# Kernel optimization log

Hardware: AMD Instinct MI355X
Metric: run time of the kernel (lower is better)

Reference implementation:

```python
import math
import jax, jax.numpy as jnp
import numpy as np


def setup_inputs() -> dict:
    key = jax.random.key(0)
    ks = jax.random.split(key, 8)
    N, Lv, M, Lt = 4096, 16, 4096, 77
    Din, D, R = 512, 768, 4  # fc in-dim, model dim, bottleneck ratio
    Dh = D // R
    s = lambda k, shape, fan_in: jax.random.normal(k, shape, jnp.float32) * (1.0 / math.sqrt(fan_in))
    return {
        "vision_prompt": jax.random.normal(ks[0], (N, Lv, D), jnp.float32),
        "text_prompt": jax.random.normal(ks[1], (M, Lt, Din), jnp.float32),
        "fc_w": s(ks[2], (D, Din), Din),        # torch Linear layout [out, in]
        "fc_b": jnp.zeros((D,), jnp.float32),
        "ln_g": jnp.ones((D,), jnp.float32),
        "ln_b": jnp.zeros((D,), jnp.float32),
        "mlp_w1": s(ks[3], (Dh, D), D),
        "mlp_b1": jnp.zeros((Dh,), jnp.float32),
        "mlp_w2": s(ks[4], (D, Dh), Dh),
        "mlp_b2": jnp.zeros((D,), jnp.float32),
    }


def _layernorm(x, g, b, eps=1e-5):
    mu = jnp.mean(x, axis=-1, keepdims=True)
    var = jnp.var(x, axis=-1, keepdims=True)
    return (x - mu) * jax.lax.rsqrt(var + eps) * g + b


def reference(vision_prompt, text_prompt, fc_w, fc_b, ln_g, ln_b,
              mlp_w1, mlp_b1, mlp_w2, mlp_b2):
    N, Lv, D = vision_prompt.shape
    mean_v = jnp.mean(vision_prompt, axis=1)                    # [N, D]
    mean_t = jnp.mean(text_prompt, axis=1)                      # [M, Din]
    t = mean_t @ fc_w.T + fc_b                                  # [M, D]
    scores = jnp.einsum('nc,mc->nm', mean_v, t) / math.sqrt(D)  # [N, M]
    aff = jax.nn.softmax(scores, axis=-1)
    agg = jnp.einsum('nm,mc->nc', aff, t)                       # [N, D]
    h = _layernorm(agg, ln_g, ln_b)
    h = jax.nn.relu(h @ mlp_w1.T + mlp_b1)
    h = h @ mlp_w2.T + mlp_b2                                   # [N, D]
    return jnp.broadcast_to(h[:, None, :], (N, Lv, D))
```

## Files before the change

### kernel.cpp

```cpp
#include <hip/hip_runtime.h>
#include <math.h>

typedef unsigned short u16;
typedef __attribute__((ext_vector_type(4))) float f32x4;
typedef __attribute__((ext_vector_type(8))) short bf16x8;

#define GLOBAL_AS __attribute__((address_space(1)))
#define LDS_AS __attribute__((address_space(3)))

__device__ __forceinline__ u16 f2bf(float f) {
  unsigned u = __builtin_bit_cast(unsigned, f);
  unsigned lsb = (u >> 16) & 1u;
  u += 0x7fffu + lsb;
  return (u16)(u >> 16);
}

__device__ __forceinline__ float bf2f(u16 b) {
  return __builtin_bit_cast(float, ((unsigned)b) << 16);
}

__device__ __forceinline__ void gload16(const void* g, void* l) {
  __builtin_amdgcn_global_load_lds((const GLOBAL_AS void*)g, (LDS_AS void*)l, 16, 0, 0);
}

__global__ __launch_bounds__(256) void prologue_kernel(
    const float* __restrict__ vision, const float* __restrict__ text,
    const float* __restrict__ fc_w, const float* __restrict__ w1,
    const float* __restrict__ w2, const float* __restrict__ b1,
    u16* __restrict__ mean_v, u16* __restrict__ mean_t,
    u16* __restrict__ fcw_bf, u16* __restrict__ w1p, u16* __restrict__ w2p,
    float* __restrict__ b1p)
{
  const int n_mv = 4096 * 192;
  const int n_mt = 4096 * 128;
  const int n_fcw = 768 * 512;
  const int n_w1 = 256 * 768;
  const int n_w2 = 768 * 256;
  int id = blockIdx.x * 256 + threadIdx.x;

  if (id < n_mv) {
    int n = id / 192, c = id % 192;
    const f32x4* x = (const f32x4*)vision + (size_t)n * 16 * 192 + c;
    f32x4 s = {0.f, 0.f, 0.f, 0.f};
#pragma unroll
    for (int l = 0; l < 16; ++l) s += __builtin_nontemporal_load(&x[(size_t)l * 192]);
    s *= (1.f / 16.f);
    ushort4 o; o.x = f2bf(s.x); o.y = f2bf(s.y); o.z = f2bf(s.z); o.w = f2bf(s.w);
    ((ushort4*)mean_v)[id] = o;
    return;
  }
  id -= n_mv;
  if (id < n_mt) {
    int n = id / 128, c = id % 128;
    const f32x4* x = (const f32x4*)text + (size_t)n * 77 * 128 + c;
    f32x4 s = {0.f, 0.f, 0.f, 0.f};
#pragma unroll 11
    for (int l = 0; l < 77; ++l) s += __builtin_nontemporal_load(&x[(size_t)l * 128]);
    s *= (1.f / 77.f);
    ushort4 o; o.x = f2bf(s.x); o.y = f2bf(s.y); o.z = f2bf(s.z); o.w = f2bf(s.w);
    ((ushort4*)mean_t)[id] = o;
    return;
  }
  id -= n_mt;
  if (id < n_fcw) { fcw_bf[id] = f2bf(fc_w[id]); return; }
  id -= n_fcw;
  if (id < n_w1) {
    int r = id / 768;
    w1p[id] = (r < 192) ? f2bf(w1[id]) : (u16)0;
    return;
  }
  id -= n_w1;
  if (id < n_w2) {
    int r = id / 256, c = id % 256;
    w2p[id] = (c < 192) ? f2bf(w2[(size_t)r * 192 + c]) : (u16)0;
    return;
  }
  id -= n_w2;
  if (id < 256) b1p[id] = (id < 192) ? b1[id] : 0.f;
}

__global__ __launch_bounds__(512, 2) void gemm256_exp_bf16(
    const u16* __restrict__ A, const u16* __restrict__ B, float alpha,
    u16* __restrict__ C, float* __restrict__ dsum, int N, int K, int lda, int ldb)
{
  __shared__ char lds[98304];
  const int tid = threadIdx.x;
  const int w = tid >> 6, lane = tid & 63;

  const int gx = gridDim.x;
  const int nb = gx * gridDim.y;
  int b0 = blockIdx.y * gx + blockIdx.x;
  int swz = (b0 & 7) * (nb >> 3) + (b0 >> 3);
  const int bx = swz % gx, by = swz / gx;
  const int brow = by * 256, bcol = bx * 256;
  const int wr = w >> 2, wc = w & 3;

  f32x4 acc[8][4];
#pragma unroll
  for (int i = 0; i < 8; ++i)
#pragma unroll
    for (int j = 0; j < 4; ++j) acc[i][j] = (f32x4){0.f, 0.f, 0.f, 0.f};

  const int srow = lane >> 2;
  const int scol = (lane & 3) * 8;
  const size_t ga0 = (size_t)(brow + (w * 2 + 0) * 16 + srow) * lda + scol;
  const size_t ga1 = (size_t)(brow + (w * 2 + 1) * 16 + srow) * lda + scol;
  const size_t gb0 = (size_t)(bcol + (w * 2 + 0) * 16 + srow) * ldb + scol;
  const size_t gb1 = (size_t)(bcol + (w * 2 + 1) * 16 + srow) * ldb + scol;

  const int fr = lane & 15, fk = (lane >> 4) * 8;
  const int NT = K >> 5;

  auto stage = [&](int ti, int b) {
    const int k0 = ti << 5;
    char* la = lds + b * 16384 + w * 2048;
    char* lb = lds + 49152 + b * 16384 + w * 2048;
    gload16(A + ga0 + k0, la);
    gload16(A + ga1 + k0, la + 1024);
    gload16(B + gb0 + k0, lb);
    gload16(B + gb1 + k0, lb + 1024);
  };

  stage(0, 0);
  stage(1, 1);

  int bR = 0;
  for (int it = 0; it < NT; ++it) {
    if (it + 1 < NT) { asm volatile("s_waitcnt vmcnt(4)" ::: "memory"); }
    else             { asm volatile("s_waitcnt vmcnt(0)" ::: "memory"); }
    __builtin_amdgcn_s_barrier();
    asm volatile("" ::: "memory");

    int bW = bR + 2; if (bW >= 3) bW -= 3;
    if (it + 2 < NT) stage(it + 2, bW);

    const u16* la = (const u16*)(lds + bR * 16384);
    const u16* lb = (const u16*)(lds + 49152 + bR * 16384);
    bf16x8 av[8], bv[4];
#pragma unroll
    for (int mi = 0; mi < 8; ++mi)
      av[mi] = *(const bf16x8*)&la[(wr * 128 + mi * 16 + fr) * 32 + fk];
#pragma unroll
    for (int ni = 0; ni < 4; ++ni)
      bv[ni] = *(const bf16x8*)&lb[(wc * 64 + ni * 16 + fr) * 32 + fk];

    __builtin_amdgcn_s_setprio(1);
#pragma unroll
    for (int mi = 0; mi < 8; ++mi)
#pragma unroll
      for (int ni = 0; ni < 4; ++ni)
        acc[mi][ni] = __builtin_amdgcn_mfma_f32_16x16x32_bf16(av[mi], bv[ni], acc[mi][ni], 0, 0, 0);
    __builtin_amdgcn_s_setprio(0);

    bR = (bR + 1 == 3) ? 0 : bR + 1;
  }

  const int fq = lane >> 4;
  __syncthreads();

  float rsum[8][4];
#pragma unroll
  for (int mi = 0; mi < 8; ++mi) {
#pragma unroll
    for (int r = 0; r < 4; ++r) rsum[mi][r] = 0.f;
#pragma unroll
    for (int ni = 0; ni < 4; ++ni)
#pragma unroll
      for (int r = 0; r < 4; ++r) {
        float v = __expf(acc[mi][ni][r] * alpha);
        acc[mi][ni][r] = v;
        rsum[mi][r] += v;
      }
  }
#pragma unroll
  for (int mi = 0; mi < 8; ++mi)
#pragma unroll
    for (int r = 0; r < 4; ++r) {
      float s = rsum[mi][r];
      s += __shfl_xor(s, 1); s += __shfl_xor(s, 2);
      s += __shfl_xor(s, 4); s += __shfl_xor(s, 8);
      rsum[mi][r] = s;
    }
  float* wsum = (float*)(lds + 73728);
  if (fr == 0) {
#pragma unroll
    for (int mi = 0; mi < 8; ++mi)
#pragma unroll
      for (int r = 0; r < 4; ++r)
        wsum[wc * 256 + wr * 128 + mi * 16 + fq * 4 + r] = rsum[mi][r];
  }

  u16* tile = (u16*)lds;
#pragma unroll
  for (int s = 0; s < 2; ++s) {
    if ((wc >> 1) == s) {
#pragma unroll
      for (int mi = 0; mi < 8; ++mi)
#pragma unroll
        for (int ni = 0; ni < 4; ++ni) {
          int cc = (wc & 1) * 64 + ni * 16 + fr;
#pragma unroll
          for (int r = 0; r < 4; ++r) {
            int rr = wr * 128 + mi * 16 + fq * 4 + r;
            tile[rr * 136 + cc] = f2bf(acc[mi][ni][r]);
          }
        }
    }
    __syncthreads();
    {
      int row = tid >> 1, part = tid & 1;
      size_t base = (size_t)(brow + row) * N + bcol + s * 128 + part * 64;
      const u16* tr = &tile[row * 136 + part * 64];
#pragma unroll
      for (int j = 0; j < 8; ++j)
        *(bf16x8*)&C[base + j * 8] = *(const bf16x8*)&tr[j * 8];
    }
    __syncthreads();
  }

  if (tid < 256) {
    float s = wsum[tid] + wsum[256 + tid] + wsum[512 + tid] + wsum[768 + tid];
    dsum[(size_t)(brow + tid) * 16 + bx] = s;
  }
}

template<bool RELU, bool BF16OUT, bool TRANST, bool BCAST16>
__global__ __launch_bounds__(256) void gemm_nt(
    const u16* __restrict__ A, const u16* __restrict__ B,
    const float* __restrict__ bias, float alpha,
    float* __restrict__ Cf, u16* __restrict__ Cb,
    u16* __restrict__ Ct, int ldt,
    int M, int N, int K, int lda, int ldb,
    int kofs, long long cofs)
{
  __shared__ char lds[49152];
  const int t = threadIdx.x;
  const int w = t >> 6, lane = t & 63;

  const int gx = gridDim.x, gy = gridDim.y;
  const int nb = gx * gy * gridDim.z;
  int b0 = (blockIdx.z * gy + blockIdx.y) * gx + blockIdx.x;
  int swz = (b0 & 7) * (nb >> 3) + (b0 >> 3);
  const int bx = swz % gx;
  int tmp = swz / gx;
  const int by = tmp % gy, kz = tmp / gy;

  const int brow = by * 128, bcol = bx * 128;
  const int wr = w >> 1, wc = w & 1;

  A += (size_t)kz * kofs;
  B += (size_t)kz * kofs;
  Cf += kz * cofs;

  f32x4 acc[4][4];
#pragma unroll
  for (int i = 0; i < 4; ++i)
#pragma unroll
    for (int j = 0; j < 4; ++j) acc[i][j] = (f32x4){0.f, 0.f, 0.f, 0.f};

  const int srow = t >> 2;
  const int scol = (t & 3) * 8;
  const size_t aoff0 = (size_t)(brow + srow) * lda + scol;
  const size_t boff0 = (size_t)(bcol + srow) * ldb + scol;
  const size_t aoff1 = aoff0 + (size_t)64 * lda;
  const size_t boff1 = boff0 + (size_t)64 * ldb;

  const int fr = lane & 15, fk = (lane >> 4) * 8;
  const int NT = K >> 5;

  auto stage = [&](int ti, int b) {
    const int k0 = ti << 5;
    char* la = lds + b * 16384 + w * 1024;
    char* lb = lds + b * 16384 + 8192 + w * 1024;
    gload16(A + aoff0 + k0, la);
    gload16(A + aoff1 + k0, la + 4096);
    gload16(B + boff0 + k0, lb);
    gload16(B + boff1 + k0, lb + 4096);
  };

  stage(0, 0);
  stage(1, 1);

  int bR = 0;
  for (int it = 0; it < NT; ++it) {
    if (it + 1 < NT) { asm volatile("s_waitcnt vmcnt(4)" ::: "memory"); }
    else             { asm volatile("s_waitcnt vmcnt(0)" ::: "memory"); }
    __builtin_amdgcn_s_barrier();
    asm volatile("" ::: "memory");

    int bW = bR + 2; if (bW >= 3) bW -= 3;
    if (it + 2 < NT) stage(it + 2, bW);

    const u16* la = (const u16*)(lds + bR * 16384);
    const u16* lb = (const u16*)(lds + bR * 16384 + 8192);
    bf16x8 av[4], bv[4];
#pragma unroll
    for (int mi = 0; mi < 4; ++mi)
      av[mi] = *(const bf16x8*)&la[(wr * 64 + mi * 16 + fr) * 32 + fk];
#pragma unroll
    for (int ni = 0; ni < 4; ++ni)
      bv[ni] = *(const bf16x8*)&lb[(wc * 64 + ni * 16 + fr) * 32 + fk];

    __builtin_amdgcn_s_setprio(1);
#pragma unroll
    for (int mi = 0; mi < 4; ++mi)
#pragma unroll
      for (int ni = 0; ni < 4; ++ni)
        acc[mi][ni] = __builtin_amdgcn_mfma_f32_16x16x32_bf16(av[mi], bv[ni], acc[mi][ni], 0, 0, 0);
    __builtin_amdgcn_s_setprio(0);

    bR = (bR + 1 == 3) ? 0 : bR + 1;
  }

  const int fq = lane >> 4;
  u16* tileT = (u16*)lds;
  if (TRANST) __syncthreads();

#pragma unroll
  for (int mi = 0; mi < 4; ++mi) {
#pragma unroll
    for (int ni = 0; ni < 4; ++ni) {
      int cl = wc * 64 + ni * 16 + fr;
      int col = bcol + cl;
      float bb = bias ? bias[col] : 0.f;
#pragma unroll
      for (int r = 0; r < 4; ++r) {
        int rl = wr * 64 + mi * 16 + fq * 4 + r;
        int row = brow + rl;
        float v = acc[mi][ni][r] * alpha + bb;
        if (RELU) v = fmaxf(v, 0.f);
        if (BF16OUT) {
          u16 bf = f2bf(v);
          Cb[(size_t)row * N + col] = bf;
          if (TRANST) tileT[cl * 130 + rl] = bf;
        } else if (BCAST16) {
          size_t b0o = ((size_t)row * 16) * (size_t)N + col;
#pragma unroll
          for (int l = 0; l < 16; ++l)
            __builtin_nontemporal_store(v, &Cf[b0o + (size_t)l * N]);
        } else {
          Cf[(size_t)row * N + col] = v;
        }
      }
    }
  }

  if (TRANST) {
    __syncthreads();
    int c2 = t >> 1, off = (t & 1) * 64;
    size_t base = (size_t)(bcol + c2) * ldt + brow + off;
#pragma unroll
    for (int j = 0; j < 8; ++j)
      *(bf16x8*)&Ct[base + j * 8] = *(const bf16x8*)&tileT[c2 * 130 + off + j * 8];
  }
}

__global__ __launch_bounds__(256) void ln2_kernel(
    const float* __restrict__ X, long long ps, const float* __restrict__ dsum,
    const float* __restrict__ g, const float* __restrict__ b,
    u16* __restrict__ Y)
{
  __shared__ float red[4];
  int row = blockIdx.x, t = threadIdx.x;
  const float* x = X + (size_t)row * 768;
  const f32x4* dv = (const f32x4*)(dsum + (size_t)row * 16);
  f32x4 d4 = dv[0] + dv[1] + dv[2] + dv[3];
  float inv_d = 1.f / (d4.x + d4.y + d4.z + d4.w);

  float v0 = (x[t]       + x[ps + t])       * inv_d;
  float v1 = (x[t + 256] + x[ps + t + 256]) * inv_d;
  float v2 = (x[t + 512] + x[ps + t + 512]) * inv_d;

  float s = v0 + v1 + v2;
#pragma unroll
  for (int off = 32; off > 0; off >>= 1) s += __shfl_xor(s, off);
  if ((t & 63) == 0) red[t >> 6] = s;
  __syncthreads();
  float mu = (red[0] + red[1] + red[2] + red[3]) * (1.f / 768.f);
  __syncthreads();

  float d0 = v0 - mu, d1 = v1 - mu, d2 = v2 - mu;
  float q = d0 * d0 + d1 * d1 + d2 * d2;
#pragma unroll
  for (int off = 32; off > 0; off >>= 1) q += __shfl_xor(q, off);
  if ((t & 63) == 0) red[t >> 6] = q;
  __syncthreads();
  float var = (red[0] + red[1] + red[2] + red[3]) * (1.f / 768.f);
  float inv = rsqrtf(var + 1e-5f);

  u16* y = Y + (size_t)row * 768;
  y[t]       = f2bf(d0 * inv * g[t]       + b[t]);
  y[t + 256] = f2bf(d1 * inv * g[t + 256] + b[t + 256]);
  y[t + 512] = f2bf(d2 * inv * g[t + 512] + b[t + 512]);
}

extern "C" void kernel_launch(void* const* d_in, const int* in_sizes, int n_in,
                              void* d_out, int out_size, void* d_ws, size_t ws_size,
                              hipStream_t stream)
{
  const float* vision = (const float*)d_in[0];
  const float* text   = (const float*)d_in[1];
  const float* fc_w   = (const float*)d_in[2];
  const float* fc_b   = (const float*)d_in[3];
  const float* ln_g   = (const float*)d_in[4];
  const float* ln_b   = (const float*)d_in[5];
  const float* w1     = (const float*)d_in[6];
  const float* b1     = (const float*)d_in[7];
  const float* w2     = (const float*)d_in[8];
  const float* b2     = (const float*)d_in[9];
  float* out = (float*)d_out;

  const int N = 4096, M = 4096, Din = 512, D = 768, Dhp = 256;

  char* p = (char*)d_ws;
  auto alloc = [&](size_t bytes) { char* r = p; p += (bytes + 255) & ~(size_t)255; return r; };
  u16*   mean_v = (u16*)alloc((size_t)N * D * 2);
  u16*   mean_t = (u16*)alloc((size_t)M * Din * 2);
  u16*   fcw_bf = (u16*)alloc((size_t)D * Din * 2);
  u16*   w1p    = (u16*)alloc((size_t)Dhp * D * 2);
  u16*   w2p    = (u16*)alloc((size_t)D * Dhp * 2);
  float* b1p    = (float*)alloc((size_t)Dhp * 4);
  float* dsum   = (float*)alloc((size_t)N * 16 * 4);
  u16*   t_bf   = (u16*)alloc((size_t)M * D * 2);
  u16*   tT_bf  = (u16*)alloc((size_t)D * M * 2);
  u16*   aff    = (u16*)alloc((size_t)N * M * 2);
  u16*   ln_o   = (u16*)alloc((size_t)N * D * 2);
  u16*   h1     = (u16*)alloc((size_t)N * Dhp * 2);
  float* aggp   = (float*)alloc((size_t)2 * N * D * 4);

  {
    int total = 4096 * 192 + 4096 * 128 + 768 * 512 + 256 * 768 + 768 * 256 + 256;
    prologue_kernel<<<(total + 255) / 256, 256, 0, stream>>>(
        vision, text, fc_w, w1, w2, b1, mean_v, mean_t, fcw_bf, w1p, w2p, b1p);
  }

  gemm_nt<false, true, true, false><<<dim3(D / 128, M / 128), 256, 0, stream>>>(
      mean_t, fcw_bf, fc_b, 1.f, nullptr, t_bf, tT_bf, M, M, D, Din, Din, Din, 0, 0);

  gemm256_exp_bf16<<<dim3(M / 256, N / 256), 512, 0, stream>>>(
      mean_v, t_bf, 1.f / sqrtf(768.f), aff, dsum, M, D, D, D);

  gemm_nt<false, false, false, false><<<dim3(D / 128, N / 128, 2), 256, 0, stream>>>(
      aff, tT_bf, nullptr, 1.f, aggp, nullptr, nullptr, 0, N, D, M / 2, M, M,
      M / 2, (long long)N * D);

  ln2_kernel<<<N, 256, 0, stream>>>(aggp, (long long)N * D, dsum, ln_g, ln_b, ln_o);

  gemm_nt<true, true, false, false><<<dim3(Dhp / 128, N / 128), 256, 0, stream>>>(
      ln_o, w1p, b1p, 1.f, nullptr, h1, nullptr, 0, N, Dhp, D, D, D, 0, 0);

  gemm_nt<false, false, false, true><<<dim3(D / 128, N / 128), 256, 0, stream>>>(
      h1, w2p, b2, 1.f, out, nullptr, nullptr, 0, N, D, Dhp, Dhp, Dhp, 0, 0);
}
```

Measured before the change: 331.4 us.

## Move 16x broadcast out of GEMM epilogue into vectorized broadcast kernel

The final MLP GEMM no longer writes each output element 16 times with scalar nontemporal stores. It writes a compact [N,D] fp32 result into the reused affinity buffer, and a separate kernel then expands it with 16-byte nontemporal vector stores. The gemm_nt kernel also gets a launch-bounds occupancy hint of 3 blocks per SM. The aim is wider, coalesced stores for the 200MB output, at the cost of one extra launch and an extra read of the compact result.

```diff
diff --git a/kernel.cpp b/kernel.cpp
--- a/kernel.cpp
+++ b/kernel.cpp
@@ -224,8 +224,8 @@
   }
 }
 
-template<bool RELU, bool BF16OUT, bool TRANST, bool BCAST16>
-__global__ __launch_bounds__(256) void gemm_nt(
+template<bool RELU, bool BF16OUT, bool TRANST>
+__global__ __launch_bounds__(256, 3) void gemm_nt(
     const u16* __restrict__ A, const u16* __restrict__ B,
     const float* __restrict__ bias, float alpha,
     float* __restrict__ Cf, u16* __restrict__ Cb,
@@ -333,11 +333,6 @@
           u16 bf = f2bf(v);
           Cb[(size_t)row * N + col] = bf;
           if (TRANST) tileT[cl * 130 + rl] = bf;
-        } else if (BCAST16) {
-          size_t b0o = ((size_t)row * 16) * (size_t)N + col;
-#pragma unroll
-          for (int l = 0; l < 16; ++l)
-            __builtin_nontemporal_store(v, &Cf[b0o + (size_t)l * N]);
         } else {
           Cf[(size_t)row * N + col] = v;
         }
@@ -392,6 +387,17 @@
   y[t]       = f2bf(d0 * inv * g[t]       + b[t]);
   y[t + 256] = f2bf(d1 * inv * g[t + 256] + b[t + 256]);
   y[t + 512] = f2bf(d2 * inv * g[t + 512] + b[t + 512]);
+}
+
+__global__ __launch_bounds__(256) void bcast_kernel(
+    const f32x4* __restrict__ H, f32x4* __restrict__ O, int total)
+{
+  int id = blockIdx.x * 256 + threadIdx.x;
+  if (id >= total) return;
+  int n = id / (16 * 192);
+  int c = id % 192;
+  f32x4 v = H[(size_t)n * 192 + c];
+  __builtin_nontemporal_store(v, &O[id]);
 }
 
 extern "C" void kernel_launch(void* const* d_in, const int* in_sizes, int n_in,
@@ -427,6 +433,7 @@
   u16*   ln_o   = (u16*)alloc((size_t)N * D * 2);
   u16*   h1     = (u16*)alloc((size_t)N * Dhp * 2);
   float* aggp   = (float*)alloc((size_t)2 * N * D * 4);
+  float* h2     = (float*)aff;
 
   {
     int total = 4096 * 192 + 4096 * 128 + 768 * 512 + 256 * 768 + 768 * 256 + 256;
@@ -434,21 +441,27 @@
         vision, text, fc_w, w1, w2, b1, mean_v, mean_t, fcw_bf, w1p, w2p, b1p);
   }
 
-  gemm_nt<false, true, true, false><<<dim3(D / 128, M / 128), 256, 0, stream>>>(
+  gemm_nt<false, true, true><<<dim3(D / 128, M / 128), 256, 0, stream>>>(
       mean_t, fcw_bf, fc_b, 1.f, nullptr, t_bf, tT_bf, M, M, D, Din, Din, Din, 0, 0);
 
   gemm256_exp_bf16<<<dim3(M / 256, N / 256), 512, 0, stream>>>(
       mean_v, t_bf, 1.f / sqrtf(768.f), aff, dsum, M, D, D, D);
 
-  gemm_nt<false, false, false, false><<<dim3(D / 128, N / 128, 2), 256, 0, stream>>>(
+  gemm_nt<false, false, false><<<dim3(D / 128, N / 128, 2), 256, 0, stream>>>(
       aff, tT_bf, nullptr, 1.f, aggp, nullptr, nullptr, 0, N, D, M / 2, M, M,
       M / 2, (long long)N * D);
 
   ln2_kernel<<<N, 256, 0, stream>>>(aggp, (long long)N * D, dsum, ln_g, ln_b, ln_o);
 
-  gemm_nt<true, true, false, false><<<dim3(Dhp / 128, N / 128), 256, 0, stream>>>(
+  gemm_nt<true, true, false><<<dim3(Dhp / 128, N / 128), 256, 0, stream>>>(
       ln_o, w1p, b1p, 1.f, nullptr, h1, nullptr, 0, N, Dhp, D, D, D, 0, 0);
 
-  gemm_nt<false, false, false, true><<<dim3(D / 128, N / 128), 256, 0, stream>>>(
-      h1, w2p, b2, 1.f, out, nullptr, nullptr, 0, N, D, Dhp, Dhp, Dhp, 0, 0);
-}
+  gemm_nt<false, false, false><<<dim3(D / 128, N / 128), 256, 0, stream>>>(
+      h1, w2p, b2, 1.f, h2, nullptr, nullptr, 0, N, D, Dhp, Dhp, Dhp, 0, 0);
+
+  {
+    int total4 = N * 16 * (D / 4);
+    bcast_kernel<<<(total4 + 255) / 256, 256, 0, stream>>>(
+        (const f32x4*)h2, (f32x4*)out, total4);
+  }
+}
```

Result: faster. 320.0 us (-3.4%).

## Stage broadcast epilogue through LDS for 16-byte coalesced output stores

Applied to the files above, without the earlier changes.

For the broadcast-16 final GEMM, the accumulator tile is staged in LDS in two 64-row halves. Each output row is then written 16 times with vectorized f32x4 non-temporal stores that are contiguous across threads, replacing the scattered scalar stores of the old epilogue. The change also adds a min-blocks-per-CU hint of 3 to the launch bounds, which may limit registers for every GEMM variant. The output width of 192 float4s is hardcoded, so it assumes N equals 768.

```diff
diff --git a/kernel.cpp b/kernel.cpp
--- a/kernel.cpp
+++ b/kernel.cpp
@@ -225,7 +225,7 @@
 }
 
 template<bool RELU, bool BF16OUT, bool TRANST, bool BCAST16>
-__global__ __launch_bounds__(256) void gemm_nt(
+__global__ __launch_bounds__(256, 3) void gemm_nt(
     const u16* __restrict__ A, const u16* __restrict__ B,
     const float* __restrict__ bias, float alpha,
     float* __restrict__ Cf, u16* __restrict__ Cb,
@@ -313,6 +313,42 @@
   }
 
   const int fq = lane >> 4;
+
+  if (BCAST16) {
+    float* tf = (float*)lds;
+#pragma unroll
+    for (int s = 0; s < 2; ++s) {
+      __syncthreads();
+      if (wr == s) {
+#pragma unroll
+        for (int mi = 0; mi < 4; ++mi)
+#pragma unroll
+          for (int ni = 0; ni < 4; ++ni) {
+            int cl = wc * 64 + ni * 16 + fr;
+            float bb = bias ? bias[bcol + cl] : 0.f;
+#pragma unroll
+            for (int r = 0; r < 4; ++r) {
+              int rl = mi * 16 + fq * 4 + r;
+              tf[rl * 132 + cl] = acc[mi][ni][r] * alpha + bb;
+            }
+          }
+      }
+      __syncthreads();
+      f32x4* O = (f32x4*)Cf;
+#pragma unroll 4
+      for (int p = 0; p < 128; ++p) {
+        int idx = p * 256 + t;
+        int within = idx & 31;
+        int seg = idx >> 5;
+        int l = seg & 15, rl = seg >> 4;
+        f32x4 v = *(const f32x4*)&tf[rl * 132 + within * 4];
+        size_t o4 = ((size_t)(brow + s * 64 + rl) * 16 + l) * 192 + (bcol >> 2) + within;
+        __builtin_nontemporal_store(v, &O[o4]);
+      }
+    }
+    return;
+  }
+
   u16* tileT = (u16*)lds;
   if (TRANST) __syncthreads();
 
@@ -333,11 +369,6 @@
           u16 bf = f2bf(v);
           Cb[(size_t)row * N + col] = bf;
           if (TRANST) tileT[cl * 130 + rl] = bf;
-        } else if (BCAST16) {
-          size_t b0o = ((size_t)row * 16) * (size_t)N + col;
-#pragma unroll
-          for (int l = 0; l < 16; ++l)
-            __builtin_nontemporal_store(v, &Cf[b0o + (size_t)l * N]);
         } else {
           Cf[(size_t)row * N + col] = v;
         }
```

Measured after the change: 310.1 us. -6.4%, faster.
